# Performance work log

Measured on AMD Instinct MI355X. Metric: run time of the kernel, lower is better.

Reference implementation:

```python
import jax, jax.numpy as jnp
import numpy as np

VOCAB, D, A = 50000, 200, 32
R, L, B, NNZ = 30000, 40, 10000, 300000


def setup_inputs() -> dict:
    key = jax.random.key(0)
    ks = jax.random.split(key, 12)
    historical_review = jax.random.randint(ks[0], (R, L), 0, VOCAB)
    review_positive = jax.random.normal(ks[1], (R, D), jnp.float32)
    review_negative = jax.random.normal(ks[2], (R, D), jnp.float32)
    u_rows = jax.random.randint(ks[3], (1, NNZ), 0, B)
    u_cols = jax.random.randint(ks[4], (1, NNZ), 0, R)
    user_histor_index = jnp.concatenate([u_rows, u_cols], axis=0)
    user_histor_value = jax.random.uniform(ks[5], (NNZ,), jnp.float32)
    i_rows = jax.random.randint(ks[6], (1, NNZ), 0, B)
    i_cols = jax.random.randint(ks[7], (1, NNZ), 0, R)
    item_histor_index = jnp.concatenate([i_rows, i_cols], axis=0)
    item_histor_value = jax.random.uniform(ks[8], (NNZ,), jnp.float32)
    # parameters (torch nn.Linear convention: y = x @ W.T + b)
    emb_table = jax.random.normal(ks[9], (VOCAB, D), jnp.float32) * 0.1  # frozen
    W_M = jax.random.normal(ks[10], (D, D), jnp.float32) / np.sqrt(D)
    W_W = jax.random.normal(ks[11], (A, D), jnp.float32) / np.sqrt(D)
    b_W = jnp.zeros((A,), jnp.float32)
    return {
        "historical_review": historical_review,
        "review_positive": review_positive,
        "review_negative": review_negative,
        "user_histor_index": user_histor_index,
        "user_histor_value": user_histor_value,
        "item_histor_index": item_histor_index,
        "item_histor_value": item_histor_value,
        "batch_size": B,
        "emb_table": emb_table,
        "W_M": W_M,
        "W_W": W_W,
        "b_W": b_W,
    }


def _spmm(index, value, p_t, n_rows):
    # sparse [n_rows, R] @ p_t [R, A] via gather + segment-sum
    rows, cols = index[0], index[1]
    contrib = value[:, None] * p_t[cols]  # [nnz, A]
    return jax.ops.segment_sum(contrib, rows, num_segments=n_rows)


def reference(historical_review, review_positive, review_negative,
              user_histor_index, user_histor_value,
              item_histor_index, item_histor_value,
              batch_size, emb_table, W_M, W_W, b_W):
    e_w = emb_table[historical_review]                    # [R, L, D] gather
    # dx = matmul(transform_M(e_w), y_s[...,None]) -> [R, L]
    mew = jnp.einsum('rld,ed->rle', e_w, W_M)             # transform_M
    dx = jnp.einsum('rld,rd->rl', mew, review_positive)
    ax = jax.nn.softmax(dx, axis=1)                       # softmax over words
    z_s = jnp.einsum('rld,rl->rd', e_w, ax)               # attention pooling
    p_t = z_s @ W_W.T + b_W                               # [R, A]
    user_aspect = _spmm(user_histor_index, user_histor_value, p_t, batch_size)
    item_aspect = _spmm(item_histor_index, item_histor_value, p_t, batch_size)
    return (user_aspect, item_aspect)
```

## Files before the change

kernel.cpp:

```cpp
#include <hip/hip_runtime.h>
#include <math.h>

#define VOCAB 50000
#define DD 200
#define AA 32
#define RR 30000
#define LL 40
#define BB 10000

typedef _Float16 half2_t __attribute__((ext_vector_type(2)));

static __device__ __forceinline__ unsigned short f2h(float f) {
    return __builtin_bit_cast(unsigned short, (_Float16)f);
}
static __device__ __forceinline__ float h2f(unsigned short u) {
    return (float)__builtin_bit_cast(_Float16, u);
}
static __device__ __forceinline__ float hlo(unsigned int u) {
    return (float)__builtin_bit_cast(_Float16, (unsigned short)(u & 0xFFFFu));
}
static __device__ __forceinline__ float hhi(unsigned int u) {
    return (float)__builtin_bit_cast(_Float16, (unsigned short)(u >> 16));
}
static __device__ __forceinline__ unsigned int pkh(float lo, float hi) {
    return (unsigned int)f2h(lo) | ((unsigned int)f2h(hi) << 16);
}
static __device__ __forceinline__ float dot2(unsigned int a, unsigned int b, float acc) {
#if __has_builtin(__builtin_amdgcn_fdot2)
    return __builtin_amdgcn_fdot2(__builtin_bit_cast(half2_t, a),
                                  __builtin_bit_cast(half2_t, b), acc, false);
#else
    return acc + hlo(a) * hlo(b) + hhi(a) * hhi(b);
#endif
}

__global__ __launch_bounds__(256) void cvt_f16_kernel(
    const float* __restrict__ src, unsigned short* __restrict__ dst, int n4)
{
    int i = blockIdx.x * 256 + threadIdx.x;
    if (i >= n4) return;
    float4 f = ((const float4*)src)[i];
    ushort4 u;
    u.x = f2h(f.x); u.y = f2h(f.y); u.z = f2h(f.z); u.w = f2h(f.w);
    ((ushort4*)dst)[i] = u;
}

__global__ __launch_bounds__(256) void pack_kernel(
    const float* __restrict__ WM, const float* __restrict__ WW,
    unsigned int* __restrict__ WMP, unsigned int* __restrict__ WWP)
{
    int i = blockIdx.x * 256 + threadIdx.x;
    const int NWM = (DD / 2) * DD;
    if (i < NWM) {
        int e2 = i / DD, d = i - e2 * DD;
        WMP[i] = pkh(WM[(2 * e2) * DD + d], WM[(2 * e2 + 1) * DD + d]);
    } else if (i < NWM + AA * (DD / 2)) {
        int k = i - NWM;
        int a = k / (DD / 2), c = k - a * (DD / 2);
        WWP[k] = pkh(WW[a * DD + 2 * c], WW[a * DD + 2 * c + 1]);
    }
}

__global__ __launch_bounds__(256) void v_gemm_kernel(
    const float* __restrict__ Y, const unsigned int* __restrict__ WMP,
    unsigned int* __restrict__ V16)
{
    __shared__ unsigned int yt[32 * (DD / 2)];
    const int r0 = blockIdx.x * 32;
    const int tid = threadIdx.x;

    for (int i = tid; i < 32 * 50; i += 256) {
        int j = i / 50, c = i - 50 * j;
        int r = r0 + j;
        float4 f = (r < RR) ? ((const float4*)(Y + (size_t)r * DD))[c]
                            : make_float4(0.f, 0.f, 0.f, 0.f);
        uint2 u = make_uint2(pkh(f.x, f.y), pkh(f.z, f.w));
        ((uint2*)yt)[i] = u;
    }
    __syncthreads();

    if (tid < DD) {
        float acc[32];
        #pragma unroll
        for (int j = 0; j < 32; ++j) acc[j] = 0.f;
        for (int e2 = 0; e2 < DD / 2; e2 += 2) {
            unsigned int w0 = WMP[e2 * DD + tid];
            unsigned int w1 = WMP[(e2 + 1) * DD + tid];
            #pragma unroll
            for (int j = 0; j < 32; ++j) {
                uint2 y2 = *(const uint2*)(yt + j * (DD / 2) + e2);
                acc[j] = dot2(y2.x, w0, acc[j]);
                acc[j] = dot2(y2.y, w1, acc[j]);
            }
        }
        #pragma unroll
        for (int j = 0; j < 32; ++j) {
            float partner = __shfl_xor(acc[j], 1);
            int r = r0 + j;
            if (r < RR && (tid & 1) == 0)
                V16[(size_t)r * (DD / 2) + (tid >> 1)] =
                    pkh(acc[j], partner);
        }
    }
}

__global__ __launch_bounds__(256, 8) void attn_kernel(
    const int* __restrict__ hist, const unsigned short* __restrict__ emb16,
    const unsigned int* __restrict__ V16, const unsigned int* __restrict__ WWP,
    const float* __restrict__ bW, float* __restrict__ PT)
{
    __shared__ __align__(16) unsigned short ew[LL * DD];
    __shared__ __align__(16) unsigned int vp[DD / 2];
    __shared__ float zss[4][DD];
    __shared__ float sws[4];
    __shared__ __align__(16) unsigned int zsp[DD / 2];

    const int r = blockIdx.x;
    const int tid = threadIdx.x;
    const int* hrow = hist + r * LL;

    const int i0 = tid, i1 = tid + 256, i2 = tid + 512, i3 = tid + 768;
    const int l0 = i0 / 25, c0 = i0 - 25 * l0;
    const int l1 = i1 / 25, c1 = i1 - 25 * l1;
    const int l2 = i2 / 25, c2 = i2 - 25 * l2;
    const int l3 = i3 / 25, c3 = i3 - 25 * l3;
    const bool has3 = (i3 < LL * 25);

    int w0 = hrow[l0];
    int w1 = hrow[l1];
    int w2 = hrow[l2];
    int w3 = has3 ? hrow[l3] : 0;

    uint4 q0 = ((const uint4*)(emb16 + (size_t)w0 * DD))[c0];
    uint4 q1 = ((const uint4*)(emb16 + (size_t)w1 * DD))[c1];
    uint4 q2 = ((const uint4*)(emb16 + (size_t)w2 * DD))[c2];
    uint4 q3 = has3 ? ((const uint4*)(emb16 + (size_t)w3 * DD))[c3]
                    : make_uint4(0u, 0u, 0u, 0u);
    uint4 vv = make_uint4(0u, 0u, 0u, 0u);
    if (tid < 25) vv = ((const uint4*)(V16 + (size_t)r * (DD / 2)))[tid];

    ((uint4*)ew)[i0] = q0;
    ((uint4*)ew)[i1] = q1;
    ((uint4*)ew)[i2] = q2;
    if (has3) ((uint4*)ew)[i3] = q3;
    if (tid < 25) ((uint4*)vp)[tid] = vv;
    __syncthreads();

    const int wave = tid >> 6, lane = tid & 63;
    const int half = lane >> 5, s = lane & 31;
    const bool act = (s < 25);

    uint4 vq = act ? ((const uint4*)vp)[s] : make_uint4(0u, 0u, 0u, 0u);

    float z0 = 0.f, z1 = 0.f, z2 = 0.f, z3 = 0.f,
          z4 = 0.f, z5 = 0.f, z6 = 0.f, z7 = 0.f;
    float sw = 0.f;
    #pragma unroll 1
    for (int j = 0; j < 5; ++j) {
        const int l = wave * 10 + 2 * j + half;
        float p = 0.f;
        uint4 eq = make_uint4(0u, 0u, 0u, 0u);
        if (act) {
            eq = *(const uint4*)(ew + l * DD + s * 8);
            p = dot2(eq.x, vq.x, p);
            p = dot2(eq.y, vq.y, p);
            p = dot2(eq.z, vq.z, p);
            p = dot2(eq.w, vq.w, p);
        }
        #pragma unroll
        for (int off = 16; off; off >>= 1) p += __shfl_xor(p, off);
        float wgt = __expf(p - 8.0f);
        sw += wgt;
        z0 += wgt * hlo(eq.x); z1 += wgt * hhi(eq.x);
        z2 += wgt * hlo(eq.y); z3 += wgt * hhi(eq.y);
        z4 += wgt * hlo(eq.z); z5 += wgt * hhi(eq.z);
        z6 += wgt * hlo(eq.w); z7 += wgt * hhi(eq.w);
    }

    z0 += __shfl_xor(z0, 32); z1 += __shfl_xor(z1, 32);
    z2 += __shfl_xor(z2, 32); z3 += __shfl_xor(z3, 32);
    z4 += __shfl_xor(z4, 32); z5 += __shfl_xor(z5, 32);
    z6 += __shfl_xor(z6, 32); z7 += __shfl_xor(z7, 32);
    float swt = sw + __shfl_xor(sw, 32);
    if (half == 0 && act) {
        ((float4*)zss[wave])[2 * s]     = make_float4(z0, z1, z2, z3);
        ((float4*)zss[wave])[2 * s + 1] = make_float4(z4, z5, z6, z7);
    }
    if (lane == 0) sws[wave] = swt;
    __syncthreads();

    if (tid < DD / 2) {
        float tot = sws[0] + sws[1] + sws[2] + sws[3];
        int d = 2 * tid;
        float za = (zss[0][d]     + zss[1][d]     + zss[2][d]     + zss[3][d])     / tot;
        float zb = (zss[0][d + 1] + zss[1][d + 1] + zss[2][d + 1] + zss[3][d + 1]) / tot;
        zsp[tid] = pkh(za, zb);
    }
    __syncthreads();

    {
        int a = tid >> 3, j = tid & 7;
        float acc = 0.f;
        #pragma unroll
        for (int k = 0; k < 13; ++k) {
            int c = j + 8 * k;
            if (c < DD / 2) acc = dot2(zsp[c], WWP[a * (DD / 2) + c], acc);
        }
        #pragma unroll
        for (int off = 4; off; off >>= 1) acc += __shfl_xor(acc, off);
        if (j == 0) PT[r * AA + a] = acc + bW[a];
    }
}

__global__ __launch_bounds__(256) void spmm_kernel(
    const int* __restrict__ uidx, const float* __restrict__ uval,
    const int* __restrict__ iidx, const float* __restrict__ ival,
    const float* __restrict__ PT, float* __restrict__ out, int nnz)
{
    int g = blockIdx.x * 256 + threadIdx.x;
    int n = g >> 5;
    const int* idx = uidx;
    const float* val = uval;
    float* o = out;
    if (n >= nnz) {
        n -= nnz;
        if (n >= nnz) return;
        idx = iidx; val = ival; o += BB * AA;
    }
    int a = g & 31;
    int row = idx[n];
    int col = idx[nnz + n];
    float w = val[n];
    atomicAdd(&o[row * AA + a], w * PT[col * AA + a]);
}

extern "C" void kernel_launch(void* const* d_in, const int* in_sizes, int n_in,
                              void* d_out, int out_size, void* d_ws, size_t ws_size,
                              hipStream_t stream) {
    const int*   hist = (const int*)d_in[0];
    const float* ypos = (const float*)d_in[1];
    const int*   uidx = (const int*)d_in[3];
    const float* uval = (const float*)d_in[4];
    const int*   iidx = (const int*)d_in[5];
    const float* ival = (const float*)d_in[6];
    const float* emb  = (const float*)d_in[8];
    const float* WM   = (const float*)d_in[9];
    const float* WW   = (const float*)d_in[10];
    const float* bW   = (const float*)d_in[11];

    unsigned short* emb16 = (unsigned short*)d_ws;
    unsigned int* WMP = (unsigned int*)(emb16 + (size_t)VOCAB * DD);
    unsigned int* WWP = WMP + (DD / 2) * DD;
    unsigned int* V16 = WWP + AA * (DD / 2);
    float* PT = (float*)(V16 + (size_t)RR * (DD / 2));
    float* out = (float*)d_out;

    const int nnz = in_sizes[4];

    hipMemsetAsync(d_out, 0, (size_t)out_size * sizeof(float), stream);

    cvt_f16_kernel<<<(VOCAB * DD / 4 + 255) / 256, 256, 0, stream>>>(
        emb, emb16, VOCAB * DD / 4);
    pack_kernel<<<((DD / 2) * DD + AA * (DD / 2) + 255) / 256, 256, 0, stream>>>(
        WM, WW, WMP, WWP);
    v_gemm_kernel<<<(RR + 31) / 32, 256, 0, stream>>>(ypos, WMP, V16);
    attn_kernel<<<RR, 256, 0, stream>>>(hist, emb16, V16, WWP, bW, PT);

    const int spmm_blocks = (2 * nnz * 32 + 255) / 256;
    spmm_kernel<<<spmm_blocks, 256, 0, stream>>>(uidx, uval, iidx, ival, PT, out, nnz);
}
```

Baseline: 225.6 us.

## Fuse prep kernels, alias attention shared memory, fp16 pooling, batch SpMM nonzeros

Merges the embedding fp16 conversion and weight packing into one prep kernel, saving a launch. In the attention kernel, the reduction buffers now alias the embedding shared tile to cut LDS use and raise occupancy, which needs an extra barrier. The attention-pooling accumulation now uses packed fp16 FMAs with a smaller exp shift, trading accuracy and overflow headroom for fewer instructions. The SpMM kernel has each 32-lane group handle four nonzeros through vector index and value loads, reducing thread count and index-load overhead.

After: 229.0 us. About the same (+1.5%).

```diff
diff --git a/kernel.cpp b/kernel.cpp
--- a/kernel.cpp
+++ b/kernel.cpp
@@ -12,9 +12,6 @@
 
 static __device__ __forceinline__ unsigned short f2h(float f) {
     return __builtin_bit_cast(unsigned short, (_Float16)f);
-}
-static __device__ __forceinline__ float h2f(unsigned short u) {
-    return (float)__builtin_bit_cast(_Float16, u);
 }
 static __device__ __forceinline__ float hlo(unsigned int u) {
     return (float)__builtin_bit_cast(_Float16, (unsigned short)(u & 0xFFFFu));
@@ -34,28 +31,26 @@
 #endif
 }
 
-__global__ __launch_bounds__(256) void cvt_f16_kernel(
-    const float* __restrict__ src, unsigned short* __restrict__ dst, int n4)
+#define NC4 (VOCAB * DD / 4)
+#define NWM ((DD / 2) * DD)
+#define NWW (AA * (DD / 2))
+__global__ __launch_bounds__(256) void prep_kernel(
+    const float* __restrict__ emb, const float* __restrict__ WM,
+    const float* __restrict__ WW, unsigned short* __restrict__ emb16,
+    unsigned int* __restrict__ WMP, unsigned int* __restrict__ WWP)
 {
     int i = blockIdx.x * 256 + threadIdx.x;
-    if (i >= n4) return;
-    float4 f = ((const float4*)src)[i];
-    ushort4 u;
-    u.x = f2h(f.x); u.y = f2h(f.y); u.z = f2h(f.z); u.w = f2h(f.w);
-    ((ushort4*)dst)[i] = u;
-}
-
-__global__ __launch_bounds__(256) void pack_kernel(
-    const float* __restrict__ WM, const float* __restrict__ WW,
-    unsigned int* __restrict__ WMP, unsigned int* __restrict__ WWP)
-{
-    int i = blockIdx.x * 256 + threadIdx.x;
-    const int NWM = (DD / 2) * DD;
-    if (i < NWM) {
-        int e2 = i / DD, d = i - e2 * DD;
-        WMP[i] = pkh(WM[(2 * e2) * DD + d], WM[(2 * e2 + 1) * DD + d]);
-    } else if (i < NWM + AA * (DD / 2)) {
-        int k = i - NWM;
+    if (i < NC4) {
+        float4 f = ((const float4*)emb)[i];
+        ushort4 u;
+        u.x = f2h(f.x); u.y = f2h(f.y); u.z = f2h(f.z); u.w = f2h(f.w);
+        ((ushort4*)emb16)[i] = u;
+    } else if (i < NC4 + NWM) {
+        int k = i - NC4;
+        int e2 = k / DD, d = k - e2 * DD;
+        WMP[k] = pkh(WM[(2 * e2) * DD + d], WM[(2 * e2 + 1) * DD + d]);
+    } else if (i < NC4 + NWM + NWW) {
+        int k = i - NC4 - NWM;
         int a = k / (DD / 2), c = k - a * (DD / 2);
         WWP[k] = pkh(WW[a * DD + 2 * c], WW[a * DD + 2 * c + 1]);
     }
@@ -109,11 +104,13 @@
     const unsigned int* __restrict__ V16, const unsigned int* __restrict__ WWP,
     const float* __restrict__ bW, float* __restrict__ PT)
 {
-    __shared__ __align__(16) unsigned short ew[LL * DD];
+    __shared__ __align__(16) unsigned char smem[LL * DD * 2];
     __shared__ __align__(16) unsigned int vp[DD / 2];
-    __shared__ float zss[4][DD];
-    __shared__ float sws[4];
-    __shared__ __align__(16) unsigned int zsp[DD / 2];
+
+    unsigned short* ew = (unsigned short*)smem;
+    float (*zss)[DD] = (float(*)[DD])smem;
+    float* sws = (float*)(smem + 4 * DD * 4);
+    unsigned int* zsp = (unsigned int*)(smem + 4 * DD * 4 + 16);
 
     const int r = blockIdx.x;
     const int tid = threadIdx.x;
@@ -152,8 +149,7 @@
 
     uint4 vq = act ? ((const uint4*)vp)[s] : make_uint4(0u, 0u, 0u, 0u);
 
-    float z0 = 0.f, z1 = 0.f, z2 = 0.f, z3 = 0.f,
-          z4 = 0.f, z5 = 0.f, z6 = 0.f, z7 = 0.f;
+    half2_t zp0 = (half2_t)0, zp1 = (half2_t)0, zp2 = (half2_t)0, zp3 = (half2_t)0;
     float sw = 0.f;
     #pragma unroll 1
     for (int j = 0; j < 5; ++j) {
@@ -169,14 +165,21 @@
         }
         #pragma unroll
         for (int off = 16; off; off >>= 1) p += __shfl_xor(p, off);
-        float wgt = __expf(p - 8.0f);
-        sw += wgt;
-        z0 += wgt * hlo(eq.x); z1 += wgt * hhi(eq.x);
-        z2 += wgt * hlo(eq.y); z3 += wgt * hhi(eq.y);
-        z4 += wgt * hlo(eq.z); z5 += wgt * hhi(eq.z);
-        z6 += wgt * hlo(eq.w); z7 += wgt * hhi(eq.w);
-    }
-
+        float wgt = __expf(p - 4.0f);
+        _Float16 wh = (_Float16)wgt;
+        half2_t w2; w2[0] = wh; w2[1] = wh;
+        sw += (float)wh;
+        zp0 = __builtin_bit_cast(half2_t, eq.x) * w2 + zp0;
+        zp1 = __builtin_bit_cast(half2_t, eq.y) * w2 + zp1;
+        zp2 = __builtin_bit_cast(half2_t, eq.z) * w2 + zp2;
+        zp3 = __builtin_bit_cast(half2_t, eq.w) * w2 + zp3;
+    }
+    __syncthreads();
+
+    float z0 = (float)zp0[0], z1 = (float)zp0[1];
+    float z2 = (float)zp1[0], z3 = (float)zp1[1];
+    float z4 = (float)zp2[0], z5 = (float)zp2[1];
+    float z6 = (float)zp3[0], z7 = (float)zp3[1];
     z0 += __shfl_xor(z0, 32); z1 += __shfl_xor(z1, 32);
     z2 += __shfl_xor(z2, 32); z3 += __shfl_xor(z3, 32);
     z4 += __shfl_xor(z4, 32); z5 += __shfl_xor(z5, 32);
@@ -218,20 +221,37 @@
     const float* __restrict__ PT, float* __restrict__ out, int nnz)
 {
     int g = blockIdx.x * 256 + threadIdx.x;
-    int n = g >> 5;
+    int grp = g >> 5;
+    int a = g & 31;
+    const int gpm = (nnz + 3) >> 2;
     const int* idx = uidx;
     const float* val = uval;
     float* o = out;
-    if (n >= nnz) {
-        n -= nnz;
-        if (n >= nnz) return;
+    if (grp >= gpm) {
+        grp -= gpm;
+        if (grp >= gpm) return;
         idx = iidx; val = ival; o += BB * AA;
     }
-    int a = g & 31;
-    int row = idx[n];
-    int col = idx[nnz + n];
-    float w = val[n];
-    atomicAdd(&o[row * AA + a], w * PT[col * AA + a]);
+    const int n0 = grp * 4;
+
+    if (((nnz & 3) == 0) && (n0 + 4 <= nnz)) {
+        int4   rows = *(const int4*)(idx + n0);
+        int4   cols = *(const int4*)(idx + nnz + n0);
+        float4 ws   = *(const float4*)(val + n0);
+        atomicAdd(&o[rows.x * AA + a], ws.x * PT[cols.x * AA + a]);
+        atomicAdd(&o[rows.y * AA + a], ws.y * PT[cols.y * AA + a]);
+        atomicAdd(&o[rows.z * AA + a], ws.z * PT[cols.z * AA + a]);
+        atomicAdd(&o[rows.w * AA + a], ws.w * PT[cols.w * AA + a]);
+    } else {
+        for (int k = 0; k < 4; ++k) {
+            int n = n0 + k;
+            if (n >= nnz) break;
+            int row = idx[n];
+            int col = idx[nnz + n];
+            float w = val[n];
+            atomicAdd(&o[row * AA + a], w * PT[col * AA + a]);
+        }
+    }
 }
 
 extern "C" void kernel_launch(void* const* d_in, const int* in_sizes, int n_in,
@@ -250,8 +270,8 @@
 
     unsigned short* emb16 = (unsigned short*)d_ws;
     unsigned int* WMP = (unsigned int*)(emb16 + (size_t)VOCAB * DD);
-    unsigned int* WWP = WMP + (DD / 2) * DD;
-    unsigned int* V16 = WWP + AA * (DD / 2);
+    unsigned int* WWP = WMP + NWM;
+    unsigned int* V16 = WWP + NWW;
     float* PT = (float*)(V16 + (size_t)RR * (DD / 2));
     float* out = (float*)d_out;
 
@@ -259,13 +279,12 @@
 
     hipMemsetAsync(d_out, 0, (size_t)out_size * sizeof(float), stream);
 
-    cvt_f16_kernel<<<(VOCAB * DD / 4 + 255) / 256, 256, 0, stream>>>(
-        emb, emb16, VOCAB * DD / 4);
-    pack_kernel<<<((DD / 2) * DD + AA * (DD / 2) + 255) / 256, 256, 0, stream>>>(
-        WM, WW, WMP, WWP);
+    prep_kernel<<<(NC4 + NWM + NWW + 255) / 256, 256, 0, stream>>>(
+        emb, WM, WW, emb16, WMP, WWP);
     v_gemm_kernel<<<(RR + 31) / 32, 256, 0, stream>>>(ypos, WMP, V16);
     attn_kernel<<<RR, 256, 0, stream>>>(hist, emb16, V16, WWP, bW, PT);
 
-    const int spmm_blocks = (2 * nnz * 32 + 255) / 256;
+    const int gpm = (nnz + 3) >> 2;
+    const int spmm_blocks = (2 * gpm * 32 + 255) / 256;
     spmm_kernel<<<spmm_blocks, 256, 0, stream>>>(uidx, uval, iidx, ival, PT, out, nnz);
 }
```
